# Kernel tuning notes

Measured on AMD Instinct MI355X. Metric: run time of the kernel, lower is better.

Reference implementation:

```python
import jax, jax.numpy as jnp
import numpy as np

HIDDEN = 512
HEADS = 8
HEAD_DIM = HIDDEN // HEADS   # 64
MAN_DIM = 256                # manifold_dim = hidden_dim // 2
SCALE = HEAD_DIM ** -0.5


def _c(re, im):
    return jax.lax.complex(re, im)


def setup_inputs() -> dict:
    key = jax.random.key(0)
    ks = jax.random.split(key, 13)
    def w(k, shape, fan_in):
        return (jax.random.normal(k, shape, dtype=jnp.float32) / np.sqrt(fan_in)).astype(jnp.float32)
    B, S = 2, 2048
    return {
        "x": jax.random.normal(ks[0], (B, S, HIDDEN), dtype=jnp.float32),
        "Wq_re": w(ks[1], (HIDDEN, HIDDEN), HIDDEN), "Wq_im": w(ks[2], (HIDDEN, HIDDEN), HIDDEN),
        "Wk_re": w(ks[3], (HIDDEN, HIDDEN), HIDDEN), "Wk_im": w(ks[4], (HIDDEN, HIDDEN), HIDDEN),
        "Wv_re": w(ks[5], (HIDDEN, HIDDEN), HIDDEN), "Wv_im": w(ks[6], (HIDDEN, HIDDEN), HIDDEN),
        "Wm_re": w(ks[7], (HEAD_DIM, MAN_DIM), HEAD_DIM), "Wm_im": w(ks[8], (HEAD_DIM, MAN_DIM), HEAD_DIM),
        "Wmi_re": w(ks[9], (MAN_DIM, HEAD_DIM), MAN_DIM), "Wmi_im": w(ks[10], (MAN_DIM, HEAD_DIM), MAN_DIM),
        "Wo_re": w(ks[11], (HIDDEN, HIDDEN), HIDDEN), "Wo_im": w(ks[12], (HIDDEN, HIDDEN), HIDDEN),
    }


def reference(x, Wq_re, Wq_im, Wk_re, Wk_im, Wv_re, Wv_im,
              Wm_re, Wm_im, Wmi_re, Wmi_im, Wo_re, Wo_im):
    B, S, D = x.shape
    # quantum state preparation: cast to complex, L2-normalize along last dim
    xc = x.astype(jnp.complex64)
    norm = jnp.linalg.norm(xc, axis=-1, keepdims=True)
    xc = xc / norm

    Wq, Wk, Wv = _c(Wq_re, Wq_im), _c(Wk_re, Wk_im), _c(Wv_re, Wv_im)
    Wm, Wmi, Wo = _c(Wm_re, Wm_im), _c(Wmi_re, Wmi_im), _c(Wo_re, Wo_im)

    def heads(t):  # [B,S,D] -> [B,H,S,head_dim]
        return t.reshape(B, S, HEADS, HEAD_DIM).transpose(0, 2, 1, 3)

    q = heads(xc @ Wq)
    k = heads(xc @ Wk)
    v = heads(xc @ Wv)

    # project each head onto the manifold (complex linear)
    qm = jnp.einsum('bhsd,dm->bhsm', q, Wm)
    km = jnp.einsum('bhsd,dm->bhsm', k, Wm)
    vm = jnp.einsum('bhsd,dm->bhsm', v, Wm)

    # Hermitian inner product attention scores; softmax over real part
    scores = jnp.einsum('bhqm,bhkm->bhqk', qm, jnp.conj(km)) * SCALE
    attn = jax.nn.softmax(scores.real, axis=-1).astype(jnp.complex64)

    outm = jnp.einsum('bhqk,bhkm->bhqm', attn, vm)
    out = jnp.einsum('bhsm,md->bhsd', outm, Wmi)        # back to head_dim
    out = out.transpose(0, 2, 1, 3).reshape(B, S, D)    # merge heads
    out = out @ Wo
    # return real/imag stacked as float32 (complex64 output -> [B,S,D,2])
    return jnp.stack([out.real, out.imag], axis=-1)
```

## Files before the change

### kernel.cpp

```cpp
#include <hip/hip_runtime.h>
#include <hip/hip_bf16.h>
#include <stdint.h>


typedef __attribute__((ext_vector_type(8))) short bf16x8;
typedef __attribute__((ext_vector_type(4))) float f32x4;

#define QSCALE 0.18033688011112042f

__device__ __forceinline__ unsigned short f2b(float f) {
    union { float f; unsigned int u; } v; v.f = f;
    unsigned int r = v.u + 0x7fffu + ((v.u >> 16) & 1u);
    return (unsigned short)(r >> 16);
}

__device__ __forceinline__ float b2f(short s) {
    union { float f; unsigned int u; } v;
    v.u = ((unsigned int)(unsigned short)s) << 16;
    return v.f;
}

__device__ __forceinline__ unsigned int cvtpk(float a, float b) {
    union { __hip_bfloat162 h; unsigned int u; } v;
    v.h = __float22bfloat162_rn(make_float2(a, b));
    return v.u;
}

__device__ __forceinline__ void ld16(void* lds, const void* g) {
    __builtin_amdgcn_global_load_lds(
        (__attribute__((address_space(1))) unsigned int*)(g),
        (__attribute__((address_space(3))) unsigned int*)(lds), 16, 0, 0);
}

__global__ __launch_bounds__(256) void k_prep(
        const float* __restrict__ x, unsigned short* __restrict__ xn,
        const float* __restrict__ Wq_re, const float* __restrict__ Wq_im,
        const float* __restrict__ Wk_re, const float* __restrict__ Wk_im,
        const float* __restrict__ Wv_re, const float* __restrict__ Wv_im,
        const float* __restrict__ Wm_re, const float* __restrict__ Wm_im,
        unsigned short* __restrict__ WqkvT, unsigned short* __restrict__ Bq,
        float* __restrict__ WmT_re, float* __restrict__ WmT_im) {
    __shared__ float tile[64][65];
    if (blockIdx.x < 1024) {
        int row  = blockIdx.x * 4 + (threadIdx.x >> 6);
        int lane = threadIdx.x & 63;
        const float4* xr = (const float4*)(x + (size_t)row * 512);
        float4 a = xr[lane], b = xr[lane + 64];
        float s = a.x*a.x + a.y*a.y + a.z*a.z + a.w*a.w
                + b.x*b.x + b.y*b.y + b.z*b.z + b.w*b.w;
        #pragma unroll
        for (int m = 1; m < 64; m <<= 1) s += __shfl_xor(s, m, 64);
        float inv = 1.0f / sqrtf(s);
        ushort4 o;
        o.x = f2b(a.x*inv); o.y = f2b(a.y*inv); o.z = f2b(a.z*inv); o.w = f2b(a.w*inv);
        *(ushort4*)&xn[(size_t)row*512 + lane*4] = o;
        o.x = f2b(b.x*inv); o.y = f2b(b.y*inv); o.z = f2b(b.z*inv); o.w = f2b(b.w*inv);
        *(ushort4*)&xn[(size_t)row*512 + 256 + lane*4] = o;
        return;
    }
    int bid = blockIdx.x - 1024;
    int tx = threadIdx.x & 63, ty = threadIdx.x >> 6;
    if (bid < 256) {
        int mat = bid >> 6, tl = bid & 63;
        const float* src = (mat==0)?Wk_re:(mat==1)?Wk_im:(mat==2)?Wv_re:Wv_im;
        int r0 = (tl >> 3) * 64, c0 = (tl & 7) * 64;
        #pragma unroll
        for (int i = 0; i < 16; i++) {
            int r = ty + i*4;
            tile[r][tx] = src[(size_t)(r0 + r)*512 + c0 + tx];
        }
        __syncthreads();
        int sec = 1024 + (mat >> 1)*1024, part = mat & 1;
        #pragma unroll
        for (int i = 0; i < 16; i++) {
            int r = ty + i*4;
            int rr = c0 + r, h = rr >> 6, j = rr & 63;
            WqkvT[(size_t)(sec + h*128 + part*64 + j)*512 + r0 + tx] = f2b(tile[tx][r]);
        }
    } else if (bid < 264) {
        int mat = (bid - 256) >> 2, tl = (bid - 256) & 3;
        const float* src = mat ? Wm_im : Wm_re;
        float* dst = mat ? WmT_im : WmT_re;
        int c0 = tl * 64;
        #pragma unroll
        for (int i = 0; i < 16; i++) {
            int r = ty + i*4;
            tile[r][tx] = src[(size_t)r*256 + c0 + tx];
        }
        __syncthreads();
        #pragma unroll
        for (int i = 0; i < 16; i++) {
            int r = ty + i*4;
            dst[(size_t)(c0 + r)*64 + tx] = tile[tx][r];
        }
    } else {
        int b3 = bid - 264;
        int mat = b3 >> 6, tl = b3 & 63;
        const float* src = mat ? Wq_im : Wq_re;
        #pragma unroll
        for (int i = 0; i < 16; i++) {
            int idx = tl*4096 + i*256 + threadIdx.x;
            int k = idx >> 9, col = idx & 511;
            int h = col >> 6, d = col & 63;
            Bq[(size_t)(h*512 + k)*128 + mat*64 + d] = f2b(src[(size_t)k*512 + col]);
        }
    }
}

__global__ __launch_bounds__(256) void k_gh(const float* __restrict__ Wm_re, const float* __restrict__ Wm_im,
                                            const float* __restrict__ WmT_re, const float* __restrict__ WmT_im,
                                            const float* __restrict__ Wmi_re, const float* __restrict__ Wmi_im,
                                            float* __restrict__ GH, unsigned short* __restrict__ Aq) {
    int id = blockIdx.x * 256 + threadIdx.x;
    int mat = id >> 12;
    int a = (id >> 6) & 63, c = id & 63;
    float s = 0.f;
    if (mat < 2) {
        for (int m = 0; m < 256; m++) {
            float ar = Wm_re[a*256+m], ai = Wm_im[a*256+m];
            float br = WmT_re[m*64+c], bi = WmT_im[m*64+c];
            s += (mat == 0) ? (ar*br + ai*bi) : (ai*br - ar*bi);
        }
        float sq = s * QSCALE;
        if (mat == 0) {
            Aq[c*128 + a]           = f2b(sq);
            Aq[(64+c)*128 + 64 + a] = f2b(sq);
        } else {
            Aq[(64+c)*128 + a]      = f2b(sq);
            Aq[c*128 + 64 + a]      = f2b(-sq);
        }
    } else {
        for (int m = 0; m < 256; m++) {
            float ar = Wm_re[a*256+m], ai = Wm_im[a*256+m];
            float br = Wmi_re[m*64+c], bi = Wmi_im[m*64+c];
            s += (mat == 2) ? (ar*br - ai*bi) : (ar*bi + ai*br);
        }
        GH[mat*4096 + c*64 + a] = s;
    }
}

__global__ __launch_bounds__(256) void k_packwo(
        const float* __restrict__ Wo_re,  const float* __restrict__ Wo_im,
        const float* __restrict__ GH, unsigned short* __restrict__ Wbig) {
    int id = blockIdx.x * 256 + threadIdx.x;
    int np = id >> 10, kk = id & 1023;
    int c = np >> 1, p = np & 1;
    int h = kk >> 7, pp = (kk >> 6) & 1, d = kk & 63;
    const float* HrT = GH + 2*4096;
    const float* HiT = GH + 3*4096;
    float s = 0.f;
    if (p == pp) {
        for (int j = 0; j < 64; j++) {
            float hr = HrT[j*64+d], hi = HiT[j*64+d];
            float wr = Wo_re[(size_t)(h*64+j)*512 + c];
            float wi = Wo_im[(size_t)(h*64+j)*512 + c];
            s += hr*wr - hi*wi;
        }
    } else {
        for (int j = 0; j < 64; j++) {
            float hr = HrT[j*64+d], hi = HiT[j*64+d];
            float wr = Wo_re[(size_t)(h*64+j)*512 + c];
            float wi = Wo_im[(size_t)(h*64+j)*512 + c];
            s += hr*wi + hi*wr;
        }
        if (p == 0) s = -s;
    }
    Wbig[(size_t)np*1024 + kk] = f2b(s);
}

template<int MODE, int MT, int MW>
__global__ __launch_bounds__(256, MW) void k_gemm(
        const unsigned short* __restrict__ Ain, const unsigned short* __restrict__ Btin,
        void* __restrict__ Cout, unsigned short* __restrict__ Vt, int K) {
    __shared__ __align__(16) unsigned short Al[2][MT*32];
    __shared__ __align__(16) unsigned short Bl[2][128*32];
    const int t = threadIdx.x;
    const int wave = t >> 6, lane = t & 63, quad = lane >> 4, l16 = lane & 15;
    const int wr = wave >> 1, wc = wave & 1;

    const unsigned short* A;
    const unsigned short* Bt;
    unsigned short* Cb = nullptr;
    int m0, n0;
    if (MODE == 0) {
        if (blockIdx.y < 16) {
            A = Ain; Bt = Btin;
            m0 = blockIdx.x * 128; n0 = blockIdx.y * 128;
            Cb = (unsigned short*)Cout;
        } else {
            int idx = (blockIdx.y - 16) * 32 + blockIdx.x;
            int b = idx >> 7, mt = (idx >> 4) & 7, nt = idx & 15;
            A  = Btin + 2048*512;
            Bt = Ain + (size_t)b*2048*512;
            m0 = mt * 128; n0 = nt * 128;
            Cb = Vt + (size_t)b*1024*2048;
        }
    } else {
        A = Ain; Bt = Btin;
        m0 = blockIdx.x * MT; n0 = blockIdx.y * 128;
    }

    f32x4 acc[MT/32][4] = {};
    for (int kt = 0; kt < K; kt += 64) {
        #pragma unroll
        for (int kh = 0; kh < 2; kh++)
            #pragma unroll
            for (int i = 0; i < MT/64; i++) {
                int g = t + i*256, r = g >> 2, gr = g & 3;
                ld16(&Al[kh][g*8], &A[(size_t)(m0 + r)*K + kt + kh*32 + gr*8]);
            }
        #pragma unroll
        for (int kh = 0; kh < 2; kh++)
            #pragma unroll
            for (int i = 0; i < 2; i++) {
                int g = t + i*256, r = g >> 2, gr = g & 3;
                ld16(&Bl[kh][g*8], &Bt[(size_t)(n0 + r)*K + kt + kh*32 + gr*8]);
            }
        __syncthreads();
        #pragma unroll
        for (int kh = 0; kh < 2; kh++) {
            bf16x8 af[MT/32], bfr[4];
            #pragma unroll
            for (int rt = 0; rt < MT/32; rt++)
                af[rt] = *(const bf16x8*)&Al[kh][(wr*(MT/2) + rt*16 + l16)*32 + quad*8];
            #pragma unroll
            for (int ct = 0; ct < 4; ct++)
                bfr[ct] = *(const bf16x8*)&Bl[kh][(wc*64 + ct*16 + l16)*32 + quad*8];
            #pragma unroll
            for (int rt = 0; rt < MT/32; rt++)
                #pragma unroll
                for (int ct = 0; ct < 4; ct++)
                    acc[rt][ct] = __builtin_amdgcn_mfma_f32_16x16x32_bf16(af[rt], bfr[ct], acc[rt][ct], 0, 0, 0);
        }
        __syncthreads();
    }
    #pragma unroll
    for (int rt = 0; rt < MT/32; rt++) {
        int row = m0 + wr*(MT/2) + rt*16 + quad*4;
        #pragma unroll
        for (int ct = 0; ct < 4; ct++) {
            int col = n0 + wc*64 + ct*16 + l16;
            if (MODE == 0) {
                unsigned int u01 = cvtpk(acc[rt][ct][0], acc[rt][ct][1]);
                unsigned int u23 = cvtpk(acc[rt][ct][2], acc[rt][ct][3]);
                Cb[(size_t)(row+0)*2048 + col] = (unsigned short)(u01);
                Cb[(size_t)(row+1)*2048 + col] = (unsigned short)(u01 >> 16);
                Cb[(size_t)(row+2)*2048 + col] = (unsigned short)(u23);
                Cb[(size_t)(row+3)*2048 + col] = (unsigned short)(u23 >> 16);
            } else if (MODE == 2) {
                unsigned short* Cq = (unsigned short*)Cout;
                int h = col >> 9, k = col & 511;
                unsigned int u01 = cvtpk(acc[rt][ct][0], acc[rt][ct][1]);
                unsigned int u23 = cvtpk(acc[rt][ct][2], acc[rt][ct][3]);
                Cq[(size_t)(h*128 + row + 0)*512 + k] = (unsigned short)(u01);
                Cq[(size_t)(h*128 + row + 1)*512 + k] = (unsigned short)(u01 >> 16);
                Cq[(size_t)(h*128 + row + 2)*512 + k] = (unsigned short)(u23);
                Cq[(size_t)(h*128 + row + 3)*512 + k] = (unsigned short)(u23 >> 16);
            } else {
                float* C = (float*)Cout;
                #pragma unroll
                for (int r = 0; r < 4; r++)
                    C[(size_t)(row + r)*1024 + col] = acc[rt][ct][r];
            }
        }
    }
}

__global__ __launch_bounds__(256, 2) void k_attn(
        const unsigned short* __restrict__ QK,
        const unsigned short* __restrict__ Vt,
        unsigned short* __restrict__ Opart,
        float* __restrict__ Lpart) {
    __shared__ __align__(16) unsigned short Kl[2][8192];
    __shared__ __align__(16) unsigned short Vl[2][8192];
    __shared__ __align__(16) unsigned short Pl[4608];

    const int t = threadIdx.x, w = t >> 6, lane = t & 63, quad = lane >> 4, l16 = lane & 15;
    const int quadx = quad ^ ((l16 >> 2) & 3);
    const int bh = blockIdx.x, b = bh >> 3, h = bh & 7;
    const int qb = blockIdx.y & 15, half = blockIdx.y >> 4;
    const int tok0 = b*2048 + qb*128;

    bf16x8 qf[2][4];
    #pragma unroll
    for (int rt = 0; rt < 2; rt++)
        #pragma unroll
        for (int ks = 0; ks < 4; ks++)
            qf[rt][ks] = *(const bf16x8*)&QK[(size_t)(tok0 + w*32 + rt*16 + l16)*2048 + h*128 + ks*32 + quad*8];

    const int grs = (t & 3) ^ ((t >> 4) & 3);
    const unsigned short* kp = QK + (size_t)(b*2048 + half*1024 + (t >> 2))*2048 + 1024 + h*128 + grs*8;
    const unsigned short* vp = Vt + (size_t)(b*1024 + h*128 + (t >> 2))*2048 + half*1024 + grs*8;

    f32x4 Oacc[2][8] = {};
    float ls[2][4] = {};

    #pragma unroll
    for (int i = 0; i < 4; i++) ld16(&Kl[0][(i*256 + t)*8], kp + i*32);
    #pragma unroll
    for (int i = 0; i < 4; i++) ld16(&Vl[0][(i*256 + t)*8], vp + (i & 1)*131072 + (i >> 1)*32);
    __syncthreads();

    for (int it = 0; it < 16; it++) {
        const int cur = it & 1;
        if (it < 15) {
            int kt2 = (it + 1) * 64;
            #pragma unroll
            for (int i = 0; i < 4; i++) ld16(&Kl[cur^1][(i*256 + t)*8], kp + (size_t)kt2*2048 + i*32);
            #pragma unroll
            for (int i = 0; i < 4; i++) ld16(&Vl[cur^1][(i*256 + t)*8], vp + kt2 + (i & 1)*131072 + (i >> 1)*32);
        }

        f32x4 S[2][4] = {};
        #pragma unroll
        for (int ks = 0; ks < 4; ks++) {
            #pragma unroll
            for (int ct = 0; ct < 4; ct++) {
                bf16x8 kf = *(const bf16x8*)&Kl[cur][ks*2048 + (ct*16 + l16)*32 + quadx*8];
                #pragma unroll
                for (int rt = 0; rt < 2; rt++)
                    S[rt][ct] = __builtin_amdgcn_mfma_f32_16x16x32_bf16(qf[rt][ks], kf, S[rt][ct], 0, 0, 0);
            }
        }
        #pragma unroll
        for (int ks2 = 0; ks2 < 2; ks2++) {
            #pragma unroll
            for (int rt = 0; rt < 2; rt++) {
                #pragma unroll
                for (int ct2 = 0; ct2 < 2; ct2++) {
                    int ct = ks2*2 + ct2;
                    float p0 = exp2f(S[rt][ct][0]), p1 = exp2f(S[rt][ct][1]);
                    float p2 = exp2f(S[rt][ct][2]), p3 = exp2f(S[rt][ct][3]);
                    ls[rt][0] += p0; ls[rt][1] += p1; ls[rt][2] += p2; ls[rt][3] += p3;
                    int q = w*32 + rt*16 + quad*4;
                    int base = ct2*16 + l16;
                    unsigned int u01 = cvtpk(p0, p1);
                    unsigned int u23 = cvtpk(p2, p3);
                    Pl[base + (q+0)*36] = (unsigned short)(u01);
                    Pl[base + (q+1)*36] = (unsigned short)(u01 >> 16);
                    Pl[base + (q+2)*36] = (unsigned short)(u23);
                    Pl[base + (q+3)*36] = (unsigned short)(u23 >> 16);
                }
            }
            bf16x8 pf[2];
            #pragma unroll
            for (int rt = 0; rt < 2; rt++)
                pf[rt] = *(const bf16x8*)&Pl[(w*32 + rt*16 + l16)*36 + quad*8];
            #pragma unroll
            for (int dt = 0; dt < 8; dt++) {
                bf16x8 vf = *(const bf16x8*)&Vl[cur][ks2*4096 + (dt*16 + l16)*32 + quadx*8];
                #pragma unroll
                for (int rt = 0; rt < 2; rt++)
                    Oacc[rt][dt] = __builtin_amdgcn_mfma_f32_16x16x32_bf16(pf[rt], vf, Oacc[rt][dt], 0, 0, 0);
            }
        }
        __syncthreads();
    }

    #pragma unroll
    for (int rt = 0; rt < 2; rt++)
        #pragma unroll
        for (int r = 0; r < 4; r++) {
            float s = ls[rt][r];
            #pragma unroll
            for (int m = 1; m < 16; m <<= 1) s += __shfl_xor(s, m, 64);
            ls[rt][r] = s;
        }
    unsigned short* Op = Opart + (size_t)half*4096*1024;
    float* Lp = Lpart + (size_t)half*32768;
    #pragma unroll
    for (int rt = 0; rt < 2; rt++) {
        int q = w*32 + rt*16 + quad*4;
        int tok = tok0 + q;
        float inv[4];
        #pragma unroll
        for (int r = 0; r < 4; r++) inv[r] = 1.0f / ls[rt][r];
        if (l16 == 0) {
            #pragma unroll
            for (int r = 0; r < 4; r++) Lp[(size_t)(tok + r)*8 + h] = ls[rt][r];
        }
        #pragma unroll
        for (int dt = 0; dt < 8; dt++) {
            int col = h*128 + dt*16 + l16;
            #pragma unroll
            for (int r = 0; r < 4; r++)
                Op[(size_t)(tok + r)*1024 + col] = f2b(Oacc[rt][dt][r] * inv[r]);
        }
    }
}

__global__ __launch_bounds__(256) void k_merge(const unsigned short* __restrict__ Opart,
                                               const float* __restrict__ Lpart,
                                               unsigned short* __restrict__ O) {
    int slot = blockIdx.x * 256 + threadIdx.x;
    int tok = slot >> 7, colg = slot & 127, h = colg >> 4;
    float l0 = Lpart[(size_t)tok*8 + h];
    float l1 = Lpart[32768 + (size_t)tok*8 + h];
    float inv = 1.0f / (l0 + l1);
    float w0 = l0*inv, w1 = l1*inv;
    size_t off = (size_t)tok*1024 + colg*8;
    bf16x8 a0 = *(const bf16x8*)&Opart[off];
    bf16x8 a1 = *(const bf16x8*)&Opart[4194304 + off];
    float o[8];
    #pragma unroll
    for (int j = 0; j < 8; j++)
        o[j] = w0*b2f(a0[j]) + w1*b2f(a1[j]);
    uint4 uo;
    uo.x = cvtpk(o[0], o[1]); uo.y = cvtpk(o[2], o[3]);
    uo.z = cvtpk(o[4], o[5]); uo.w = cvtpk(o[6], o[7]);
    *(uint4*)&O[off] = uo;
}

extern "C" void kernel_launch(void* const* d_in, const int* in_sizes, int n_in,
                              void* d_out, int out_size, void* d_ws, size_t ws_size,
                              hipStream_t stream) {
    (void)in_sizes; (void)n_in; (void)out_size; (void)ws_size;
    const float* x      = (const float*)d_in[0];
    const float* Wq_re  = (const float*)d_in[1];
    const float* Wq_im  = (const float*)d_in[2];
    const float* Wk_re  = (const float*)d_in[3];
    const float* Wk_im  = (const float*)d_in[4];
    const float* Wv_re  = (const float*)d_in[5];
    const float* Wv_im  = (const float*)d_in[6];
    const float* Wm_re  = (const float*)d_in[7];
    const float* Wm_im  = (const float*)d_in[8];
    const float* Wmi_re = (const float*)d_in[9];
    const float* Wmi_im = (const float*)d_in[10];
    const float* Wo_re  = (const float*)d_in[11];
    const float* Wo_im  = (const float*)d_in[12];

    char* ws = (char*)d_ws;
    unsigned short* xn    = (unsigned short*)(ws);
    unsigned short* WqkvT = (unsigned short*)(ws + (4u << 20));
    unsigned short* Wbig  = (unsigned short*)(ws + (7u << 20));
    float*          GH    = (float*)         (ws + (9u << 20));
    float*          WmT_re= (float*)         (ws + (9u << 20) + (64u << 10));
    float*          WmT_im= (float*)         (ws + (9u << 20) + (128u << 10));
    unsigned short* Aq    = (unsigned short*)(ws + (9u << 20) + (192u << 10));
    unsigned short* QK    = (unsigned short*)(ws + (10u << 20));
    unsigned short* Bq    = (unsigned short*)(ws + (10u << 20));
    unsigned short* Vt    = (unsigned short*)(ws + (26u << 20));
    unsigned short* Obuf  = (unsigned short*)(ws + (34u << 20));
    unsigned short* Opart = (unsigned short*)(ws + (42u << 20));
    float*          Lpart = (float*)         (ws + (74u << 20));

    k_prep         <<<dim3(1416), dim3(256), 0, stream>>>(
        x, xn, Wq_re, Wq_im, Wk_re, Wk_im, Wv_re, Wv_im, Wm_re, Wm_im,
        WqkvT, Bq, WmT_re, WmT_im);
    k_gh           <<<dim3(64),   dim3(256), 0, stream>>>(
        Wm_re, Wm_im, WmT_re, WmT_im, Wmi_re, Wmi_im, GH, Aq);
    k_gemm<2,128,2><<<dim3(1, 32),  dim3(256), 0, stream>>>(Aq, Bq, (void*)WqkvT, nullptr, 128);
    k_packwo       <<<dim3(4096), dim3(256), 0, stream>>>(Wo_re, Wo_im, GH, Wbig);
    k_gemm<0,128,3><<<dim3(32, 24), dim3(256), 0, stream>>>(xn, WqkvT, (void*)QK, Vt, 512);
    k_attn         <<<dim3(16, 32), dim3(256), 0, stream>>>(QK, Vt, Opart, Lpart);
    k_merge        <<<dim3(2048), dim3(256), 0, stream>>>(Opart, Lpart, Obuf);
    k_gemm<1,64,2> <<<dim3(64, 8),  dim3(256), 0, stream>>>(Obuf, Wbig, d_out, nullptr, 1024);
}
```

Baseline: 233.5 us.

## Stage GEMM epilogue through LDS for vector stores; halve attention K/V tiles for occupancy

The GEMM kernel now reuses its staging shared memory to transpose the accumulator tile, so outputs go to global memory as 16-byte vector stores instead of scattered scalar writes. The attention kernel processes 32 keys per iteration instead of 64, halving the K/V shared buffers, and raises launch bounds to 3 blocks per CU. The aim is better global write coalescing and more resident blocks. The cost is an extra LDS round trip and sync in the epilogue, and twice as many barrier iterations in attention.

```diff
diff --git a/kernel.cpp b/kernel.cpp
--- a/kernel.cpp
+++ b/kernel.cpp
@@ -172,8 +172,13 @@
 __global__ __launch_bounds__(256, MW) void k_gemm(
         const unsigned short* __restrict__ Ain, const unsigned short* __restrict__ Btin,
         void* __restrict__ Cout, unsigned short* __restrict__ Vt, int K) {
-    __shared__ __align__(16) unsigned short Al[2][MT*32];
-    __shared__ __align__(16) unsigned short Bl[2][128*32];
+    constexpr int STAGE = MT*128 + 16384;
+    constexpr int EPIL  = (MODE == 1) ? MT*128*4 : 128*128*2;
+    constexpr int SMB   = STAGE > EPIL ? STAGE : EPIL;
+    __shared__ __align__(16) char smem[SMB];
+    unsigned short* AlB = (unsigned short*)smem;
+    unsigned short* BlB = (unsigned short*)(smem + MT*128);
+
     const int t = threadIdx.x;
     const int wave = t >> 6, lane = t & 63, quad = lane >> 4, l16 = lane & 15;
     const int wr = wave >> 1, wc = wave & 1;
@@ -207,14 +212,14 @@
             #pragma unroll
             for (int i = 0; i < MT/64; i++) {
                 int g = t + i*256, r = g >> 2, gr = g & 3;
-                ld16(&Al[kh][g*8], &A[(size_t)(m0 + r)*K + kt + kh*32 + gr*8]);
+                ld16(&AlB[kh*(MT*32) + g*8], &A[(size_t)(m0 + r)*K + kt + kh*32 + gr*8]);
             }
         #pragma unroll
         for (int kh = 0; kh < 2; kh++)
             #pragma unroll
             for (int i = 0; i < 2; i++) {
                 int g = t + i*256, r = g >> 2, gr = g & 3;
-                ld16(&Bl[kh][g*8], &Bt[(size_t)(n0 + r)*K + kt + kh*32 + gr*8]);
+                ld16(&BlB[kh*4096 + g*8], &Bt[(size_t)(n0 + r)*K + kt + kh*32 + gr*8]);
             }
         __syncthreads();
         #pragma unroll
@@ -222,10 +227,10 @@
             bf16x8 af[MT/32], bfr[4];
             #pragma unroll
             for (int rt = 0; rt < MT/32; rt++)
-                af[rt] = *(const bf16x8*)&Al[kh][(wr*(MT/2) + rt*16 + l16)*32 + quad*8];
+                af[rt] = *(const bf16x8*)&AlB[kh*(MT*32) + (wr*(MT/2) + rt*16 + l16)*32 + quad*8];
             #pragma unroll
             for (int ct = 0; ct < 4; ct++)
-                bfr[ct] = *(const bf16x8*)&Bl[kh][(wc*64 + ct*16 + l16)*32 + quad*8];
+                bfr[ct] = *(const bf16x8*)&BlB[kh*4096 + (wc*64 + ct*16 + l16)*32 + quad*8];
             #pragma unroll
             for (int rt = 0; rt < MT/32; rt++)
                 #pragma unroll
@@ -234,45 +239,66 @@
         }
         __syncthreads();
     }
-    #pragma unroll
-    for (int rt = 0; rt < MT/32; rt++) {
-        int row = m0 + wr*(MT/2) + rt*16 + quad*4;
-        #pragma unroll
-        for (int ct = 0; ct < 4; ct++) {
-            int col = n0 + wc*64 + ct*16 + l16;
-            if (MODE == 0) {
+
+    if (MODE == 1) {
+        float* Sf = (float*)smem;
+        #pragma unroll
+        for (int rt = 0; rt < MT/32; rt++) {
+            int row = wr*(MT/2) + rt*16 + quad*4;
+            #pragma unroll
+            for (int ct = 0; ct < 4; ct++) {
+                int col = wc*64 + ct*16 + l16;
+                #pragma unroll
+                for (int r = 0; r < 4; r++)
+                    Sf[(row + r)*128 + col] = acc[rt][ct][r];
+            }
+        }
+        __syncthreads();
+        float* C = (float*)Cout;
+        #pragma unroll
+        for (int i = 0; i < MT/8; i++) {
+            int g = i*256 + t, row = g >> 5, cc = (g & 31)*4;
+            *(float4*)&C[(size_t)(m0 + row)*1024 + n0 + cc] = *(const float4*)&Sf[row*128 + cc];
+        }
+    } else {
+        unsigned short* Sh = (unsigned short*)smem;
+        #pragma unroll
+        for (int rt = 0; rt < MT/32; rt++) {
+            int row = wr*(MT/2) + rt*16 + quad*4;
+            #pragma unroll
+            for (int ct = 0; ct < 4; ct++) {
+                int col = wc*64 + ct*16 + l16;
                 unsigned int u01 = cvtpk(acc[rt][ct][0], acc[rt][ct][1]);
                 unsigned int u23 = cvtpk(acc[rt][ct][2], acc[rt][ct][3]);
-                Cb[(size_t)(row+0)*2048 + col] = (unsigned short)(u01);
-                Cb[(size_t)(row+1)*2048 + col] = (unsigned short)(u01 >> 16);
-                Cb[(size_t)(row+2)*2048 + col] = (unsigned short)(u23);
-                Cb[(size_t)(row+3)*2048 + col] = (unsigned short)(u23 >> 16);
-            } else if (MODE == 2) {
+                Sh[(row+0)*128 + col] = (unsigned short)(u01);
+                Sh[(row+1)*128 + col] = (unsigned short)(u01 >> 16);
+                Sh[(row+2)*128 + col] = (unsigned short)(u23);
+                Sh[(row+3)*128 + col] = (unsigned short)(u23 >> 16);
+            }
+        }
+        __syncthreads();
+        #pragma unroll
+        for (int i = 0; i < 8; i++) {
+            int g = i*256 + t, row = g >> 4, cc = (g & 15)*8;
+            bf16x8 v = *(const bf16x8*)&Sh[row*128 + cc];
+            if (MODE == 0) {
+                *(bf16x8*)&Cb[(size_t)(m0 + row)*2048 + n0 + cc] = v;
+            } else {
                 unsigned short* Cq = (unsigned short*)Cout;
-                int h = col >> 9, k = col & 511;
-                unsigned int u01 = cvtpk(acc[rt][ct][0], acc[rt][ct][1]);
-                unsigned int u23 = cvtpk(acc[rt][ct][2], acc[rt][ct][3]);
-                Cq[(size_t)(h*128 + row + 0)*512 + k] = (unsigned short)(u01);
-                Cq[(size_t)(h*128 + row + 1)*512 + k] = (unsigned short)(u01 >> 16);
-                Cq[(size_t)(h*128 + row + 2)*512 + k] = (unsigned short)(u23);
-                Cq[(size_t)(h*128 + row + 3)*512 + k] = (unsigned short)(u23 >> 16);
-            } else {
-                float* C = (float*)Cout;
-                #pragma unroll
-                for (int r = 0; r < 4; r++)
-                    C[(size_t)(row + r)*1024 + col] = acc[rt][ct][r];
-            }
-        }
-    }
-}
-
-__global__ __launch_bounds__(256, 2) void k_attn(
+                int h2 = n0 >> 9, k0 = n0 & 511;
+                *(bf16x8*)&Cq[(size_t)(h2*128 + m0 + row)*512 + k0 + cc] = v;
+            }
+        }
+    }
+}
+
+__global__ __launch_bounds__(256, 3) void k_attn(
         const unsigned short* __restrict__ QK,
         const unsigned short* __restrict__ Vt,
         unsigned short* __restrict__ Opart,
         float* __restrict__ Lpart) {
-    __shared__ __align__(16) unsigned short Kl[2][8192];
-    __shared__ __align__(16) unsigned short Vl[2][8192];
+    __shared__ __align__(16) unsigned short Kl[2][4096];
+    __shared__ __align__(16) unsigned short Vl[2][4096];
     __shared__ __align__(16) unsigned short Pl[4608];
 
     const int t = threadIdx.x, w = t >> 6, lane = t & 63, quad = lane >> 4, l16 = lane & 15;
@@ -289,70 +315,67 @@
             qf[rt][ks] = *(const bf16x8*)&QK[(size_t)(tok0 + w*32 + rt*16 + l16)*2048 + h*128 + ks*32 + quad*8];
 
     const int grs = (t & 3) ^ ((t >> 4) & 3);
-    const unsigned short* kp = QK + (size_t)(b*2048 + half*1024 + (t >> 2))*2048 + 1024 + h*128 + grs*8;
+    const unsigned short* kp = QK + (size_t)(b*2048 + half*1024 + ((t >> 2) & 31))*2048 + 1024 + h*128
+                               + (t >> 7)*32 + grs*8;
     const unsigned short* vp = Vt + (size_t)(b*1024 + h*128 + (t >> 2))*2048 + half*1024 + grs*8;
 
     f32x4 Oacc[2][8] = {};
     float ls[2][4] = {};
 
     #pragma unroll
-    for (int i = 0; i < 4; i++) ld16(&Kl[0][(i*256 + t)*8], kp + i*32);
-    #pragma unroll
-    for (int i = 0; i < 4; i++) ld16(&Vl[0][(i*256 + t)*8], vp + (i & 1)*131072 + (i >> 1)*32);
+    for (int i = 0; i < 2; i++) ld16(&Kl[0][(i*256 + t)*8], kp + i*64);
+    #pragma unroll
+    for (int i = 0; i < 2; i++) ld16(&Vl[0][(i*256 + t)*8], vp + (size_t)i*64*2048);
     __syncthreads();
 
-    for (int it = 0; it < 16; it++) {
+    for (int it = 0; it < 32; it++) {
         const int cur = it & 1;
-        if (it < 15) {
-            int kt2 = (it + 1) * 64;
-            #pragma unroll
-            for (int i = 0; i < 4; i++) ld16(&Kl[cur^1][(i*256 + t)*8], kp + (size_t)kt2*2048 + i*32);
-            #pragma unroll
-            for (int i = 0; i < 4; i++) ld16(&Vl[cur^1][(i*256 + t)*8], vp + kt2 + (i & 1)*131072 + (i >> 1)*32);
-        }
-
-        f32x4 S[2][4] = {};
+        if (it < 31) {
+            int kt2 = (it + 1) * 32;
+            #pragma unroll
+            for (int i = 0; i < 2; i++) ld16(&Kl[cur^1][(i*256 + t)*8], kp + (size_t)kt2*2048 + i*64);
+            #pragma unroll
+            for (int i = 0; i < 2; i++) ld16(&Vl[cur^1][(i*256 + t)*8], vp + kt2 + (size_t)i*64*2048);
+        }
+
+        f32x4 S[2][2] = {};
         #pragma unroll
         for (int ks = 0; ks < 4; ks++) {
             #pragma unroll
-            for (int ct = 0; ct < 4; ct++) {
-                bf16x8 kf = *(const bf16x8*)&Kl[cur][ks*2048 + (ct*16 + l16)*32 + quadx*8];
+            for (int ct = 0; ct < 2; ct++) {
+                bf16x8 kf = *(const bf16x8*)&Kl[cur][ks*1024 + (ct*16 + l16)*32 + quadx*8];
                 #pragma unroll
                 for (int rt = 0; rt < 2; rt++)
                     S[rt][ct] = __builtin_amdgcn_mfma_f32_16x16x32_bf16(qf[rt][ks], kf, S[rt][ct], 0, 0, 0);
             }
         }
         #pragma unroll
-        for (int ks2 = 0; ks2 < 2; ks2++) {
-            #pragma unroll
-            for (int rt = 0; rt < 2; rt++) {
-                #pragma unroll
-                for (int ct2 = 0; ct2 < 2; ct2++) {
-                    int ct = ks2*2 + ct2;
-                    float p0 = exp2f(S[rt][ct][0]), p1 = exp2f(S[rt][ct][1]);
-                    float p2 = exp2f(S[rt][ct][2]), p3 = exp2f(S[rt][ct][3]);
-                    ls[rt][0] += p0; ls[rt][1] += p1; ls[rt][2] += p2; ls[rt][3] += p3;
-                    int q = w*32 + rt*16 + quad*4;
-                    int base = ct2*16 + l16;
-                    unsigned int u01 = cvtpk(p0, p1);
-                    unsigned int u23 = cvtpk(p2, p3);
-                    Pl[base + (q+0)*36] = (unsigned short)(u01);
-                    Pl[base + (q+1)*36] = (unsigned short)(u01 >> 16);
-                    Pl[base + (q+2)*36] = (unsigned short)(u23);
-                    Pl[base + (q+3)*36] = (unsigned short)(u23 >> 16);
-                }
-            }
-            bf16x8 pf[2];
+        for (int rt = 0; rt < 2; rt++) {
+            #pragma unroll
+            for (int ct = 0; ct < 2; ct++) {
+                float p0 = exp2f(S[rt][ct][0]), p1 = exp2f(S[rt][ct][1]);
+                float p2 = exp2f(S[rt][ct][2]), p3 = exp2f(S[rt][ct][3]);
+                ls[rt][0] += p0; ls[rt][1] += p1; ls[rt][2] += p2; ls[rt][3] += p3;
+                int q = w*32 + rt*16 + quad*4;
+                int base = ct*16 + l16;
+                unsigned int u01 = cvtpk(p0, p1);
+                unsigned int u23 = cvtpk(p2, p3);
+                Pl[base + (q+0)*36] = (unsigned short)(u01);
+                Pl[base + (q+1)*36] = (unsigned short)(u01 >> 16);
+                Pl[base + (q+2)*36] = (unsigned short)(u23);
+                Pl[base + (q+3)*36] = (unsigned short)(u23 >> 16);
+            }
+        }
+        bf16x8 pf[2];
+        #pragma unroll
+        for (int rt = 0; rt < 2; rt++)
+            pf[rt] = *(const bf16x8*)&Pl[(w*32 + rt*16 + l16)*36 + quad*8];
+        #pragma unroll
+        for (int dt = 0; dt < 8; dt++) {
+            bf16x8 vf = *(const bf16x8*)&Vl[cur][(dt*16 + l16)*32 + quadx*8];
             #pragma unroll
             for (int rt = 0; rt < 2; rt++)
-                pf[rt] = *(const bf16x8*)&Pl[(w*32 + rt*16 + l16)*36 + quad*8];
-            #pragma unroll
-            for (int dt = 0; dt < 8; dt++) {
-                bf16x8 vf = *(const bf16x8*)&Vl[cur][ks2*4096 + (dt*16 + l16)*32 + quadx*8];
-                #pragma unroll
-                for (int rt = 0; rt < 2; rt++)
-                    Oacc[rt][dt] = __builtin_amdgcn_mfma_f32_16x16x32_bf16(pf[rt], vf, Oacc[rt][dt], 0, 0, 0);
-            }
+                Oacc[rt][dt] = __builtin_amdgcn_mfma_f32_16x16x32_bf16(pf[rt], vf, Oacc[rt][dt], 0, 0, 0);
         }
         __syncthreads();
     }
```

Result: slower. 245.1 us (+5.0%).
